# Performance work log

Hardware: AMD Instinct MI355X
Metric: run time of the kernel (lower is better)

The kernel has to match this reference:

```python
import jax, jax.numpy as jnp
import numpy as np

# Faithful reference for NeighborSample: the original builds a one-hot
# input[y+i-2, x+j-2, k] into output channel s = k*25 + i*5 + j, then
# reshapes [b,h,w,c,5,5] -> transpose -> [b*h*w,5,5,c].
# Equivalently: zero-pad by 2 and gather every 5x5 neighborhood per pixel.

def setup_inputs() -> dict:
    key = jax.random.key(0)
    x = jax.random.normal(key, (8, 64, 64, 192), dtype=jnp.float32)
    return {"x": x}


def reference(x) -> jnp.ndarray:
    b, h, w, c = x.shape
    K = 5  # neighborhood size
    pad = K // 2
    xp = jnp.pad(x, ((0, 0), (pad, pad), (pad, pad), (0, 0)))  # zero pad == conv SAME
    # 25 shifted views stacked on a new axis -> [b, h, w, 25, c]
    patches = jnp.stack(
        [xp[:, i:i + h, j:j + w, :] for i in range(K) for j in range(K)],
        axis=3,
    )
    # [b, h, w, 25, c] -> [b*h*w, 5, 5, c]
    return patches.reshape(b * h * w, K, K, c)
```

## Files before the change

kernel.cpp:

```cpp
#include <hip/hip_runtime.h>


typedef float f32x4 __attribute__((ext_vector_type(4)));

constexpr int B = 8;
constexpr int H = 64;
constexpr int W = 64;
constexpr int C4 = 48;
constexpr int K = 5;
constexpr int PAD = K / 2;
constexpr int ROW = K * K * C4;

constexpr unsigned NPIX  = (unsigned)B * H * W;
constexpr unsigned TOTAL = NPIX * C4;
constexpr int BLOCK = 256;
constexpr unsigned GRID = TOTAL / BLOCK;

__global__ __launch_bounds__(BLOCK) void neighbor_scatter_kernel(
    const f32x4* __restrict__ in, f32x4* __restrict__ out) {
  unsigned g  = blockIdx.x * BLOCK + threadIdx.x;
  unsigned k4 = g % C4;
  unsigned p  = g / C4;

  int xx = (int)(p & (W - 1));
  int yy = (int)((p >> 6) & (H - 1));

  f32x4 v = in[g];
  int pbase = (int)(p * (unsigned)ROW + k4);

  bool interior = (yy >= PAD) & (yy < H - PAD) & (xx >= PAD) & (xx < W - PAD);

  if (__all(interior)) {
#pragma unroll
    for (int oi = 0; oi < K; ++oi)
#pragma unroll
      for (int oj = 0; oj < K; ++oj) {
        const int off = ((PAD - oi) * W + (PAD - oj)) * ROW + (oi * K + oj) * C4;
        out[pbase + off] = v;
      }
  } else {
    const f32x4 z = {0.f, 0.f, 0.f, 0.f};
#pragma unroll
    for (int oi = 0; oi < K; ++oi)
#pragma unroll
      for (int oj = 0; oj < K; ++oj) {
        const int off = ((PAD - oi) * W + (PAD - oj)) * ROW + (oi * K + oj) * C4;
        int ty = yy + PAD - oi, tx = xx + PAD - oj;
        if ((unsigned)ty < (unsigned)H && (unsigned)tx < (unsigned)W)
          out[pbase + off] = v;
        int sy = yy + oi - PAD, sx = xx + oj - PAD;
        if (!((unsigned)sy < (unsigned)H && (unsigned)sx < (unsigned)W))
          out[pbase + (oi * K + oj) * C4] = z;
      }
  }
}

extern "C" void kernel_launch(void* const* d_in, const int* in_sizes, int n_in,
                              void* d_out, int out_size, void* d_ws, size_t ws_size,
                              hipStream_t stream) {
  const f32x4* in = (const f32x4*)d_in[0];
  f32x4* out = (f32x4*)d_out;
  neighbor_scatter_kernel<<<GRID, BLOCK, 0, stream>>>(in, out);
}
```

Baseline: 631.3 us.

## Stage input window in LDS and write output contiguously per pixel tile

Replaces the per-input scatter kernel with a gather kernel. Each block loads a 5-row by 20-column input window into shared memory and then streams the 16 pixels' 25-tap outputs as one contiguous region. This turns scattered strided stores into fully coalesced sequential writes, at the cost of shared-memory staging, a barrier and redundant input reads across overlapping windows.

Measured after the change: 634.2 us. No clear change (+0.4%).

```diff
diff --git a/kernel.cpp b/kernel.cpp
--- a/kernel.cpp
+++ b/kernel.cpp
@@ -11,47 +11,67 @@
 constexpr int PAD = K / 2;
 constexpr int ROW = K * K * C4;
 
-constexpr unsigned NPIX  = (unsigned)B * H * W;
-constexpr unsigned TOTAL = NPIX * C4;
+constexpr int TP   = 16;
+constexpr int WIN  = TP + 2 * PAD;
+constexpr int WROW = WIN * C4;
+constexpr int LDSF4 = K * WROW;
+constexpr int OUTF4 = TP * ROW;
+
 constexpr int BLOCK = 256;
-constexpr unsigned GRID = TOTAL / BLOCK;
+constexpr unsigned NBLK = (unsigned)B * H * (W / TP);
 
-__global__ __launch_bounds__(BLOCK) void neighbor_scatter_kernel(
+__global__ __launch_bounds__(BLOCK) void neighbor_lds_kernel(
     const f32x4* __restrict__ in, f32x4* __restrict__ out) {
-  unsigned g  = blockIdx.x * BLOCK + threadIdx.x;
-  unsigned k4 = g % C4;
-  unsigned p  = g / C4;
+  __shared__ f32x4 lds[LDSF4];
 
-  int xx = (int)(p & (W - 1));
-  int yy = (int)((p >> 6) & (H - 1));
+  const int tid = (int)threadIdx.x;
+  const unsigned blk = blockIdx.x;
+  const int xblk = (int)(blk & (W / TP - 1));
+  const int y    = (int)((blk >> 2) & (H - 1));
+  const int b    = (int)(blk >> 8);
+  const int x0   = xblk * TP;
 
-  f32x4 v = in[g];
-  int pbase = (int)(p * (unsigned)ROW + k4);
+  const bool interior =
+      (y >= PAD) & (y < H - PAD) & (x0 >= PAD) & (x0 + TP + PAD <= W);
 
-  bool interior = (yy >= PAD) & (yy < H - PAD) & (xx >= PAD) & (xx < W - PAD);
+  if (interior) {
+    const f32x4* src = in + ((b * H + (y - PAD)) * W + (x0 - PAD)) * C4;
+    for (int i = tid; i < LDSF4; i += BLOCK) {
+      int r   = i / WROW;
+      int rem = i - r * WROW;
+      lds[i] = src[r * (W * C4) + rem];
+    }
+  } else {
+    for (int i = tid; i < LDSF4; i += BLOCK) {
+      int r   = i / WROW;
+      int rem = i - r * WROW;
+      int col = rem / C4;
+      int k4  = rem - col * C4;
+      int ys = y + r - PAD;
+      int xs = x0 + col - PAD;
+      f32x4 v = {0.f, 0.f, 0.f, 0.f};
+      if ((unsigned)ys < (unsigned)H && (unsigned)xs < (unsigned)W)
+        v = in[((b * H + ys) * W + xs) * C4 + k4];
+      lds[i] = v;
+    }
+  }
+  __syncthreads();
 
-  if (__all(interior)) {
-#pragma unroll
-    for (int oi = 0; oi < K; ++oi)
-#pragma unroll
-      for (int oj = 0; oj < K; ++oj) {
-        const int off = ((PAD - oi) * W + (PAD - oj)) * ROW + (oi * K + oj) * C4;
-        out[pbase + off] = v;
-      }
-  } else {
-    const f32x4 z = {0.f, 0.f, 0.f, 0.f};
-#pragma unroll
-    for (int oi = 0; oi < K; ++oi)
-#pragma unroll
-      for (int oj = 0; oj < K; ++oj) {
-        const int off = ((PAD - oi) * W + (PAD - oj)) * ROW + (oi * K + oj) * C4;
-        int ty = yy + PAD - oi, tx = xx + PAD - oj;
-        if ((unsigned)ty < (unsigned)H && (unsigned)tx < (unsigned)W)
-          out[pbase + off] = v;
-        int sy = yy + oi - PAD, sx = xx + oj - PAD;
-        if (!((unsigned)sy < (unsigned)H && (unsigned)sx < (unsigned)W))
-          out[pbase + (oi * K + oj) * C4] = z;
-      }
+  f32x4* dst = out + (size_t)((b * H + y) * W + x0) * ROW;
+
+  int tap = tid / C4;
+  int k4  = tid - tap * C4;
+  int pl  = 0;
+
+#pragma unroll 5
+  for (int j = tid; j < OUTF4; j += BLOCK) {
+    int oi = (tap * 205) >> 10;
+    int oj = tap - oi * 5;
+    dst[j] = lds[(oi * WIN + pl + oj) * C4 + k4];
+    k4  += BLOCK % C4;
+    tap += BLOCK / C4;
+    if (k4 >= C4)   { k4 -= C4; ++tap; }
+    if (tap >= K*K) { tap -= K*K; ++pl; }
   }
 }
 
@@ -60,5 +80,5 @@
                               hipStream_t stream) {
   const f32x4* in = (const f32x4*)d_in[0];
   f32x4* out = (f32x4*)d_out;
-  neighbor_scatter_kernel<<<GRID, BLOCK, 0, stream>>>(in, out);
+  neighbor_lds_kernel<<<NBLK, BLOCK, 0, stream>>>(in, out);
 }
```

## Switch from input-scatter to output-ordered gather with grid-stride loop

Applied to the files above, without the earlier changes.

Each thread now writes contiguous output float4s in output order and gathers the matching input element (or zero for padding), instead of each input element being scattered to 25 strided output locations. This makes the dominant write traffic fully sequential and coalesced and drops the separate zero-fill branch. In exchange, input is reread about 25 times (mostly from cache), and every output element pays integer divisions to decode its index. A fixed 1024-block grid-stride loop replaces one thread per input vector.

Result: slower. 689.3 us (+9.2%).

```diff
diff --git a/kernel.cpp b/kernel.cpp
--- a/kernel.cpp
+++ b/kernel.cpp
@@ -12,46 +12,36 @@
 constexpr int ROW = K * K * C4;
 
 constexpr unsigned NPIX  = (unsigned)B * H * W;
-constexpr unsigned TOTAL = NPIX * C4;
+constexpr unsigned TOTF4 = NPIX * ROW;
 constexpr int BLOCK = 256;
-constexpr unsigned GRID = TOTAL / BLOCK;
+constexpr unsigned GRID = 1024;
+constexpr unsigned STRIDE = GRID * BLOCK;
+constexpr int ITERS = (int)(TOTF4 / STRIDE);
 
-__global__ __launch_bounds__(BLOCK) void neighbor_scatter_kernel(
+__global__ __launch_bounds__(BLOCK) void neighbor_fillorder_kernel(
     const f32x4* __restrict__ in, f32x4* __restrict__ out) {
-  unsigned g  = blockIdx.x * BLOCK + threadIdx.x;
-  unsigned k4 = g % C4;
-  unsigned p  = g / C4;
+  unsigned j = blockIdx.x * BLOCK + threadIdx.x;
 
-  int xx = (int)(p & (W - 1));
-  int yy = (int)((p >> 6) & (H - 1));
+#pragma unroll 5
+  for (int it = 0; it < ITERS; ++it, j += STRIDE) {
+    unsigned p   = j / 1200u;
+    unsigned r   = j - p * 1200u;
+    unsigned tap = r / 48u;
+    unsigned k4  = r - tap * 48u;
+    unsigned oi  = tap / 5u;
+    unsigned oj  = tap - oi * 5u;
 
-  f32x4 v = in[g];
-  int pbase = (int)(p * (unsigned)ROW + k4);
+    int x = (int)(p & (W - 1));
+    int y = (int)((p >> 6) & (H - 1));
+    int b = (int)(p >> 12);
+    int sy = y + (int)oi - PAD;
+    int sx = x + (int)oj - PAD;
 
-  bool interior = (yy >= PAD) & (yy < H - PAD) & (xx >= PAD) & (xx < W - PAD);
+    f32x4 v = {0.f, 0.f, 0.f, 0.f};
+    if ((unsigned)sy < (unsigned)H && (unsigned)sx < (unsigned)W)
+      v = in[((unsigned)(b * H + sy) * W + (unsigned)sx) * C4 + k4];
 
-  if (__all(interior)) {
-#pragma unroll
-    for (int oi = 0; oi < K; ++oi)
-#pragma unroll
-      for (int oj = 0; oj < K; ++oj) {
-        const int off = ((PAD - oi) * W + (PAD - oj)) * ROW + (oi * K + oj) * C4;
-        out[pbase + off] = v;
-      }
-  } else {
-    const f32x4 z = {0.f, 0.f, 0.f, 0.f};
-#pragma unroll
-    for (int oi = 0; oi < K; ++oi)
-#pragma unroll
-      for (int oj = 0; oj < K; ++oj) {
-        const int off = ((PAD - oi) * W + (PAD - oj)) * ROW + (oi * K + oj) * C4;
-        int ty = yy + PAD - oi, tx = xx + PAD - oj;
-        if ((unsigned)ty < (unsigned)H && (unsigned)tx < (unsigned)W)
-          out[pbase + off] = v;
-        int sy = yy + oi - PAD, sx = xx + oj - PAD;
-        if (!((unsigned)sy < (unsigned)H && (unsigned)sx < (unsigned)W))
-          out[pbase + (oi * K + oj) * C4] = z;
-      }
+    out[j] = v;
   }
 }
 
@@ -60,5 +50,5 @@
                               hipStream_t stream) {
   const f32x4* in = (const f32x4*)d_in[0];
   f32x4* out = (f32x4*)d_out;
-  neighbor_scatter_kernel<<<GRID, BLOCK, 0, stream>>>(in, out);
+  neighbor_fillorder_kernel<<<GRID, BLOCK, 0, stream>>>(in, out);
 }
```
